# Optimization experiments

Measured on AMD Instinct MI355X. Metric: run time of the kernel, lower is better.

Reference implementation:

```python
import jax, jax.numpy as jnp
import numpy as np

DIM = 2048; N_HEADS = 16; Q_RANK = 1536; KV_RANK = 192
NOPE = 128; ROPE = 64; QK_HD = NOPE + ROPE  # 192 == KV_RANK (required by k_norm/cache widths)
B = 2; S = 2048; MAX_SEQ = 2048
EPS = 1e-6
SCALE = QK_HD ** -0.5


def _rms(v, w):
    return v * jax.lax.rsqrt(jnp.mean(v * v, axis=-1, keepdims=True) + EPS) * w


def _rope(v, cos, sin):
    # v: [..., d] with interleaved (even, odd) pairs, cos/sin broadcastable to [..., d//2]
    vr = v.reshape(v.shape[:-1] + (-1, 2))
    a, b = vr[..., 0], vr[..., 1]
    return jnp.stack([a * cos - b * sin, a * sin + b * cos], axis=-1).reshape(v.shape)


def setup_inputs() -> dict:
    key = jax.random.key(0)
    ks = jax.random.split(key, 8)
    std = 0.02
    x = jax.random.normal(ks[0], (B, S, DIM), jnp.float32)
    # rotary tables: [S, ROPE//2, 2] = (cos, sin)
    t = jnp.arange(S, dtype=jnp.float32)
    inv = 1.0 / (10000.0 ** (jnp.arange(0, ROPE, 2, dtype=jnp.float32) / ROPE))
    ang = jnp.outer(t, inv)
    freqs_cis = jnp.stack([jnp.cos(ang), jnp.sin(ang)], axis=-1)
    mask = jnp.triu(jnp.full((S, S), -1e9, jnp.float32), k=1)  # causal additive mask
    c_kv_cache = jnp.zeros((B, MAX_SEQ, KV_RANK), jnp.float32)
    return {
        "x": x, "start_pos": 0, "freqs_cis": freqs_cis, "mask": mask,
        "c_kv_cache": c_kv_cache,
        "wqa_w": jax.random.normal(ks[1], (Q_RANK, DIM), jnp.float32) * std,
        "wqa_b": jnp.zeros((Q_RANK,), jnp.float32),
        "wqb_w": jax.random.normal(ks[2], (N_HEADS * QK_HD, Q_RANK), jnp.float32) * std,
        "wqb_b": jnp.zeros((N_HEADS * QK_HD,), jnp.float32),
        "q_norm_w": jnp.ones((Q_RANK,), jnp.float32),
        "wkva_w": jax.random.normal(ks[3], (QK_HD, DIM), jnp.float32) * std,
        "wkva_b": jnp.zeros((QK_HD,), jnp.float32),
        "k_norm_w": jnp.ones((KV_RANK,), jnp.float32),
        "wuk_w": jax.random.normal(ks[4], (NOPE, NOPE), jnp.float32) * std,
        "wuk_b": jnp.zeros((NOPE,), jnp.float32),
        "wuv_w": jax.random.normal(ks[5], (DIM, NOPE), jnp.float32) * std,
        "wuv_b": jnp.zeros((DIM,), jnp.float32),
    }


def reference(x, start_pos, freqs_cis, mask, c_kv_cache,
              wqa_w, wqa_b, wqb_w, wqb_b, q_norm_w,
              wkva_w, wkva_b, k_norm_w, wuk_w, wuk_b, wuv_w, wuv_b):
    bsz, seqlen, _ = x.shape
    end = start_pos + seqlen
    cos, sin = freqs_cis[..., 0], freqs_cis[..., 1]  # [seqlen, ROPE//2]

    # low-rank Q path: down-proj -> RMSNorm -> up-proj -> per-head split
    q = _rms(x @ wqa_w.T + wqa_b, q_norm_w)
    q = (q @ wqb_w.T + wqb_b).reshape(bsz, seqlen, N_HEADS, QK_HD)
    q_nope, q_pe = q[..., :NOPE], q[..., NOPE:]
    q_pe = _rope(q_pe, cos[None, :, None, :], sin[None, :, None, :])

    # latent KV path: project -> RMSNorm -> partial RoPE -> scatter into cache
    kv = _rms(x @ wkva_w.T + wkva_b, k_norm_w)  # [b, s, KV_RANK]
    k_pe = _rope(kv[..., NOPE:], cos[None, :, :], sin[None, :, :])
    kv = jnp.concatenate([kv[..., :NOPE], k_pe], axis=-1)
    cache = jax.lax.dynamic_update_slice(c_kv_cache, kv, (0, start_pos, 0))
    keys = cache[:bsz, :end]  # [b, t, KV_RANK]
    k_nope, k_rope = keys[..., :NOPE], keys[..., NOPE:]

    # absorbed attention: fold w_uk into the query side, attend in latent space
    q_abs = q_nope @ wuk_w.T + wuk_b  # [b, s, h, NOPE]
    scores = (jnp.einsum('bshd,btd->bsht', q_abs, k_nope)
              + jnp.einsum('bshr,btr->bsht', q_pe, k_rope)) * SCALE
    scores = scores + mask[None, :seqlen, None, :end]
    attn = jax.nn.softmax(scores, axis=-1)
    out = jnp.einsum('bsht,btd->bshd', attn, k_nope)  # latent values
    out = (out @ wuv_w.T + wuv_b).sum(axis=2)  # up-project values, merge heads -> [b, s, dim]
    return out
```

## Files before the change

### kernel.cpp

```cpp
#include <hip/hip_runtime.h>
#include <hip/hip_bf16.h>
#include <stdint.h>

#define NH     16
#define QRANK  1536
#define NOPE_  128
#define QKHD   192
#define NMERGE 1728
#define B_     2
#define S_     2048
#define MAXSEQ 2048
#define EPS_   1e-6f
#define SCALE_ 0.07216878364870322f

typedef __attribute__((ext_vector_type(4))) float f32x4;
typedef __attribute__((ext_vector_type(8))) short short8;
typedef __attribute__((ext_vector_type(4))) short short4v;

__device__ inline short f2bf(float f){
  uint32_t u = __builtin_bit_cast(uint32_t, f);
  uint32_t r = (u + 0x7FFFu + ((u >> 16) & 1u)) >> 16;
  return (short)(uint16_t)r;
}
__device__ inline float bf2f(short s){
  uint32_t u = ((uint32_t)(uint16_t)s) << 16;
  return __builtin_bit_cast(float, u);
}
__device__ inline void gload16(const short* g, short* l){
  __builtin_amdgcn_global_load_lds((const __attribute__((address_space(1))) void*)g,
                                   (__attribute__((address_space(3))) void*)l, 16, 0, 0);
}

__global__ void k_f2b(const float* __restrict__ in, short* __restrict__ out, long n){
  long i = ((long)blockIdx.x * blockDim.x + threadIdx.x) * 4;
  long stride = (long)gridDim.x * blockDim.x * 4;
  for(; i < n; i += stride){
    float4 v = *reinterpret_cast<const float4*>(in + i);
    short4v o;
    o.x = f2bf(v.x); o.y = f2bf(v.y); o.z = f2bf(v.z); o.w = f2bf(v.w);
    *reinterpret_cast<short4v*>(out + i) = o;
  }
}

template<int BN, bool OUT_BF16>
__global__ __launch_bounds__(256)
void k_gemm97(const short* __restrict__ A, const short* __restrict__ Bm,
              const float* __restrict__ bias, float biasScale,
              void* __restrict__ Cp, int M, int N, int K, int ldc)
{
  constexpr int WN = BN / 2, FN = WN / 16;
  __shared__ short As[128 * 32];
  __shared__ short Bs[BN * 32];
  const int tid = threadIdx.x;
  const int l = tid & 63, w = tid >> 6;
  const int wr = w >> 1, wc = w & 1;
  const long m0 = (long)blockIdx.x * 128;
  const long n0 = (long)blockIdx.y * BN;
  const int lrow = l & 15, lk8 = (l >> 4) * 8;

  int ciA0 = (w*2 + 0)*64 + l, ciA1 = (w*2 + 1)*64 + l;
  const short* a0 = &A[(m0 + (ciA0 >> 2))*(long)K + (ciA0 & 3)*8];
  const short* a1 = &A[(m0 + (ciA1 >> 2))*(long)K + (ciA1 & 3)*8];
  short* lA0 = &As[(w*2 + 0)*512];
  short* lA1 = &As[(w*2 + 1)*512];

  const short* b0; const short* b1 = nullptr;
  short* lB0; short* lB1 = nullptr;
  if constexpr (BN == 128){
    int ciB0 = (w*2 + 0)*64 + l, ciB1 = (w*2 + 1)*64 + l;
    b0 = &Bm[(n0 + (ciB0 >> 2))*(long)K + (ciB0 & 3)*8];
    b1 = &Bm[(n0 + (ciB1 >> 2))*(long)K + (ciB1 & 3)*8];
    lB0 = &Bs[(w*2 + 0)*512];
    lB1 = &Bs[(w*2 + 1)*512];
  } else {
    int ciB = w*64 + l;
    b0 = &Bm[(n0 + (ciB >> 2))*(long)K + (ciB & 3)*8];
    lB0 = &Bs[w*512];
  }

  f32x4 acc[4][FN];
  #pragma unroll
  for(int m = 0; m < 4; m++)
    #pragma unroll
    for(int n = 0; n < FN; n++) acc[m][n] = (f32x4)0.0f;

  for(int kt = 0; kt < K; kt += 32){
    gload16(a0 + kt, lA0);
    gload16(a1 + kt, lA1);
    gload16(b0 + kt, lB0);
    if constexpr (BN == 128) gload16(b1 + kt, lB1);
    __syncthreads();
    short8 af[4], bfv[FN];
    #pragma unroll
    for(int m = 0; m < 4; m++)
      af[m] = *reinterpret_cast<const short8*>(&As[(wr*64 + m*16 + lrow)*32 + lk8]);
    #pragma unroll
    for(int n = 0; n < FN; n++)
      bfv[n] = *reinterpret_cast<const short8*>(&Bs[(wc*WN + n*16 + lrow)*32 + lk8]);
    #pragma unroll
    for(int m = 0; m < 4; m++)
      #pragma unroll
      for(int n = 0; n < FN; n++)
        acc[m][n] = __builtin_amdgcn_mfma_f32_16x16x32_bf16(af[m], bfv[n], acc[m][n], 0, 0, 0);
    __syncthreads();
  }
  #pragma unroll
  for(int m = 0; m < 4; m++){
    int row_l = wr*64 + m*16 + (l >> 4)*4;
    #pragma unroll
    for(int n = 0; n < FN; n++){
      int col = (int)n0 + wc*WN + n*16 + lrow;
      float bv = bias ? bias[col]*biasScale : 0.0f;
      #pragma unroll
      for(int r = 0; r < 4; r++){
        long row = m0 + row_l + r;
        float v = acc[m][n][r] + bv;
        if constexpr (OUT_BF16) ((short*)Cp)[row*(long)ldc + col] = f2bf(v);
        else                    ((float*)Cp)[row*(long)ldc + col] = v;
      }
    }
  }
}

__global__ __launch_bounds__(256)
void k_rms_q(const float* __restrict__ in, const float* __restrict__ bias,
             const float* __restrict__ w, short* __restrict__ out)
{
  const int row = blockIdx.x;
  const int tid = threadIdx.x;
  const float* p = in + (long)row * NMERGE;
  float v[6]; float ss = 0.0f;
  #pragma unroll
  for(int i = 0; i < 6; i++){
    int c = tid + 256*i;
    v[i] = p[c] + bias[c];
    ss += v[i]*v[i];
  }
  #pragma unroll
  for(int off = 1; off < 64; off <<= 1) ss += __shfl_xor(ss, off);
  __shared__ float red[4];
  if((tid & 63) == 0) red[tid >> 6] = ss;
  __syncthreads();
  ss = red[0] + red[1] + red[2] + red[3];
  float scale = rsqrtf(ss / (float)QRANK + EPS_);
  #pragma unroll
  for(int i = 0; i < 6; i++){
    int c = tid + 256*i;
    out[(long)row*QRANK + c] = f2bf(v[i] * scale * w[c]);
  }
}

__global__ __launch_bounds__(256)
void k_qassemble(const short* __restrict__ q, const float* __restrict__ freqs,
                 short* __restrict__ qn, short* __restrict__ qfull)
{
  long idx = (long)blockIdx.x*256 + threadIdx.x;
  long hr = idx / 48; int r = (int)(idx % 48);
  long bs = hr >> 4; int h = (int)(hr & 15);
  int s = (int)(bs & (S_ - 1));
  if(r < 32){
    short4v v = *reinterpret_cast<const short4v*>(&q[bs*3072 + h*QKHD + r*4]);
    *reinterpret_cast<short4v*>(&qn[hr*128 + r*4]) = v;
  } else {
    int c = r - 32;
    short4v v = *reinterpret_cast<const short4v*>(&q[bs*3072 + h*QKHD + 128 + c*4]);
    float a0 = bf2f(v.x), b0 = bf2f(v.y), a1 = bf2f(v.z), b1 = bf2f(v.w);
    int p0 = s*32 + c*2, p1 = p0 + 1;
    float cs0 = freqs[p0*2], sn0 = freqs[p0*2 + 1];
    float cs1 = freqs[p1*2], sn1 = freqs[p1*2 + 1];
    short4v o;
    o.x = f2bf(a0*cs0 - b0*sn0); o.y = f2bf(a0*sn0 + b0*cs0);
    o.z = f2bf(a1*cs1 - b1*sn1); o.w = f2bf(a1*sn1 + b1*cs1);
    *reinterpret_cast<short4v*>(&qfull[hr*QKHD + 128 + c*4]) = o;
  }
}

__global__ __launch_bounds__(256)
void k_kvproc(const float* __restrict__ kvf, const float* __restrict__ kvb,
              const float* __restrict__ w, const float* __restrict__ freqs,
              const float* __restrict__ cache, const int* __restrict__ sp_ptr,
              short* __restrict__ kf)
{
  int wid = threadIdx.x >> 6, l = threadIdx.x & 63;
  long row = (long)blockIdx.x*4 + wid;
  int b = (int)(row >> 11);
  int t = (int)(row & (MAXSEQ - 1));
  int sp = sp_ptr[0];
  int end = sp + S_;
  if(t < sp){
    const float* c = cache + row*QKHD;
    kf[row*QKHD + l]       = f2bf(c[l]);
    kf[row*QKHD + 64 + l]  = f2bf(c[64 + l]);
    kf[row*QKHD + 128 + l] = f2bf(c[128 + l]);
    return;
  }
  if(t >= end) return;
  int s = t - sp;
  const float* p = kvf + ((long)b*S_ + s)*NMERGE;
  float v0 = p[l] + kvb[l];
  float v1 = p[64 + l] + kvb[64 + l];
  float v2 = p[128 + l] + kvb[128 + l];
  float ss = v0*v0 + v1*v1 + v2*v2;
  #pragma unroll
  for(int off = 1; off < 64; off <<= 1) ss += __shfl_xor(ss, off);
  float scale = rsqrtf(ss / (float)QKHD + EPS_);
  float n0 = v0*scale*w[l], n1 = v1*scale*w[64 + l], n2 = v2*scale*w[128 + l];
  kf[row*QKHD + l]      = f2bf(n0);
  kf[row*QKHD + 64 + l] = f2bf(n1);
  int i = l >> 1;
  float cs = freqs[(s*32 + i)*2], sn = freqs[(s*32 + i)*2 + 1];
  float pv = __shfl_xor(n2, 1);
  float r = (l & 1) ? (pv*sn + n2*cs) : (n2*cs - pv*sn);
  kf[row*QKHD + 128 + l] = f2bf(r);
}

__global__ __launch_bounds__(256)
void k_vtrans(const short* __restrict__ kf, short* __restrict__ vt)
{
  __shared__ short T[32 * 132];
  const int b = blockIdx.y;
  const int t0 = blockIdx.x * 32;
  const int tid = threadIdx.x;
  #pragma unroll
  for(int i = 0; i < 4; i++){
    int c = tid + 256*i;
    int tr = c >> 5, dg = c & 31;
    short4v v = *reinterpret_cast<const short4v*>(&kf[((long)b*MAXSEQ + t0 + tr)*QKHD + dg*4]);
    *reinterpret_cast<short4v*>(&T[tr*132 + dg*4]) = v;
  }
  __syncthreads();
  #pragma unroll
  for(int i = 0; i < 4; i++){
    int c = tid + 256*i;
    int dr = c >> 3, tg = c & 7;
    short4v v;
    v.x = T[(tg*4 + 0)*132 + dr];
    v.y = T[(tg*4 + 1)*132 + dr];
    v.z = T[(tg*4 + 2)*132 + dr];
    v.w = T[(tg*4 + 3)*132 + dr];
    *reinterpret_cast<short4v*>(&vt[((long)b*128 + dr)*MAXSEQ + t0 + tg*4]) = v;
  }
}

__global__ __launch_bounds__(256, 4)
void k_attn6(const short* __restrict__ qfull, const short* __restrict__ kf,
             const short* __restrict__ vt, const int* __restrict__ sp_ptr,
             short* __restrict__ oh)
{
  __shared__ short Ks[64 * 192];
  __shared__ short Ps[4][16 * 68];
  const int tid = threadIdx.x;
  const int l = tid & 63, w = tid >> 6;
  const int lrow = l & 15, lhi = l >> 4;
  const int bid = blockIdx.x;
  const int g = bid >> 8, kk = (bid >> 5) & 7, hb = bid & 31;
  const int tile = (g < 2) ? (31 - 8*g - kk) : (8*(3 - g) + kk);
  const int h = hb & 15, b = hb >> 4;
  const int sp = sp_ptr[0];
  const long kbase = (long)b * MAXSEQ;
  const long vbase = (long)b * 128;
  const int q0 = tile * 64;

  short8 kreg[6];

  short8 qa[6];
  {
    int s = q0 + w*16 + lrow;
    const short* qp = qfull + (((long)b*S_ + s)*NH + h)*QKHD + lhi*8;
    #pragma unroll
    for(int ks = 0; ks < 6; ks++) qa[ks] = *reinterpret_cast<const short8*>(qp + ks*32);
  }
  f32x4 o[8];
  #pragma unroll
  for(int df = 0; df < 8; df++) o[df] = (f32x4)0.0f;
  float mrun[4], lrun[4];
  #pragma unroll
  for(int i = 0; i < 4; i++){ mrun[i] = -1e30f; lrun[i] = 0.0f; }

  int hi = q0 + 64 + sp;
  int nt = (hi + 63) >> 6; if(nt > (MAXSEQ >> 6)) nt = MAXSEQ >> 6;

  {
    #pragma unroll
    for(int i = 0; i < 6; i++){
      int cid = tid + 256*i;  int r = cid/24, c = cid%24;
      kreg[i] = *reinterpret_cast<const short8*>(&kf[(kbase + r)*QKHD + c*8]);
    }
    #pragma unroll
    for(int i = 0; i < 6; i++){
      int cid = tid + 256*i;  int r = cid/24, c = cid%24;
      *reinterpret_cast<short8*>(&Ks[r*192 + (c ^ (r & 7))*8]) = kreg[i];
    }
  }
  __syncthreads();

  for(int t0 = 0; t0 < nt; t0++){
    const int T0 = t0 * 64;
    if(t0 + 1 < nt){
      const int Tn = T0 + 64;
      #pragma unroll
      for(int i = 0; i < 6; i++){
        int cid = tid + 256*i;  int r = cid/24, c = cid%24;
        kreg[i] = *reinterpret_cast<const short8*>(&kf[(kbase + Tn + r)*QKHD + c*8]);
      }
    }
    f32x4 sc[4];
    #pragma unroll
    for(int tf = 0; tf < 4; tf++) sc[tf] = (f32x4)0.0f;
    #pragma unroll
    for(int ks = 0; ks < 6; ks++){
      #pragma unroll
      for(int tf = 0; tf < 4; tf++){
        int krow = tf*16 + lrow;
        int cs = (ks*4 + lhi) ^ (lrow & 7);
        short8 bfr = *reinterpret_cast<const short8*>(&Ks[krow*192 + cs*8]);
        sc[tf] = __builtin_amdgcn_mfma_f32_16x16x32_bf16(qa[ks], bfr, sc[tf], 0, 0, 0);
      }
    }
    const bool needmask = (T0 + 63 > q0 + w*16 + sp);
    #pragma unroll
    for(int rr = 0; rr < 4; rr++){
      int q = q0 + w*16 + lhi*4 + rr;
      float s0 = sc[0][rr]*SCALE_, s1 = sc[1][rr]*SCALE_;
      float s2 = sc[2][rr]*SCALE_, s3 = sc[3][rr]*SCALE_;
      if(needmask){
        int t = T0 + lrow;
        if(t      > q + sp) s0 = -1e30f;
        if(t + 16 > q + sp) s1 = -1e30f;
        if(t + 32 > q + sp) s2 = -1e30f;
        if(t + 48 > q + sp) s3 = -1e30f;
      }
      float mx = fmaxf(fmaxf(s0, s1), fmaxf(s2, s3));
      #pragma unroll
      for(int off = 1; off < 16; off <<= 1) mx = fmaxf(mx, __shfl_xor(mx, off));
      if(mx > mrun[rr] + 8.0f){
        float corr = __expf(mrun[rr] - mx);
        lrun[rr] *= corr;
        #pragma unroll
        for(int df = 0; df < 8; df++) o[df][rr] *= corr;
        mrun[rr] = mx;
      }
      float p0 = __expf(s0 - mrun[rr]), p1 = __expf(s1 - mrun[rr]);
      float p2 = __expf(s2 - mrun[rr]), p3 = __expf(s3 - mrun[rr]);
      float psum = (p0 + p1) + (p2 + p3);
      #pragma unroll
      for(int off = 1; off < 16; off <<= 1) psum += __shfl_xor(psum, off);
      lrun[rr] += psum;
      int prow = lhi*4 + rr;
      Ps[w][prow*68 + lrow]      = f2bf(p0);
      Ps[w][prow*68 + 16 + lrow] = f2bf(p1);
      Ps[w][prow*68 + 32 + lrow] = f2bf(p2);
      Ps[w][prow*68 + 48 + lrow] = f2bf(p3);
    }
    short8 pa[2];
    #pragma unroll
    for(int kc = 0; kc < 2; kc++)
      pa[kc] = *reinterpret_cast<const short8*>(&Ps[w][lrow*68 + kc*32 + lhi*8]);
    #pragma unroll
    for(int df = 0; df < 8; df++){
      #pragma unroll
      for(int kc = 0; kc < 2; kc++){
        short8 vfr = *reinterpret_cast<const short8*>(
            &vt[(vbase + df*16 + lrow)*MAXSEQ + T0 + kc*32 + lhi*8]);
        o[df] = __builtin_amdgcn_mfma_f32_16x16x32_bf16(pa[kc], vfr, o[df], 0, 0, 0);
      }
    }
    __syncthreads();
    if(t0 + 1 < nt){
      #pragma unroll
      for(int i = 0; i < 6; i++){
        int cid = tid + 256*i;  int r = cid/24, c = cid%24;
        *reinterpret_cast<short8*>(&Ks[r*192 + (c ^ (r & 7))*8]) = kreg[i];
      }
      __syncthreads();
    }
  }
  #pragma unroll
  for(int rr = 0; rr < 4; rr++){
    int s = q0 + w*16 + lhi*4 + rr;
    float inv = 1.0f / lrun[rr];
    #pragma unroll
    for(int df = 0; df < 8; df++)
      oh[(((long)b*S_ + s)*NH + h)*128 + df*16 + lrow] = f2bf(o[df][rr] * inv);
  }
}

__global__ __launch_bounds__(256)
void k_redheads(const short* __restrict__ ohp, short* __restrict__ hs){
  long idx = (long)blockIdx.x*256 + threadIdx.x;
  long row = idx >> 5; int d4 = (int)(idx & 31);
  float a0 = 0, a1 = 0, a2 = 0, a3 = 0;
  #pragma unroll
  for(int h = 0; h < NH; h++){
    short4v v = *reinterpret_cast<const short4v*>(&ohp[(row*NH + h)*128 + d4*4]);
    a0 += bf2f(v.x); a1 += bf2f(v.y); a2 += bf2f(v.z); a3 += bf2f(v.w);
  }
  short4v o; o.x = f2bf(a0); o.y = f2bf(a1); o.z = f2bf(a2); o.w = f2bf(a3);
  *reinterpret_cast<short4v*>(&hs[row*128 + d4*4]) = o;
}

static constexpr size_t OFF_X16   = 0;
static constexpr size_t OFF_WQAKV = 16777216;
static constexpr size_t OFF_WQB   = 23855104;
static constexpr size_t OFF_WUK   = 33292288;
static constexpr size_t OFF_WUV   = 33325056;
static constexpr size_t OFF_QNORM = 33849344;
static constexpr size_t OFF_QFULL = 46432256;
static constexpr size_t OFF_KFULL = 71598080;
static constexpr size_t OFF_HSUM  = 73170944;
static constexpr size_t OFF_SCR   = 74219520;
static constexpr size_t OFF_QAKV  = OFF_SCR;
static constexpr size_t OFF_Q16   = OFF_SCR;
static constexpr size_t OFF_QN    = OFF_SCR + 25165824;
static constexpr size_t OFF_OH    = OFF_SCR;
static constexpr size_t OFF_VT    = OFF_SCR + 41943040;

extern "C" void kernel_launch(void* const* d_in, const int* in_sizes, int n_in,
                              void* d_out, int out_size, void* d_ws, size_t ws_size,
                              hipStream_t stream)
{
  const float* x      = (const float*)d_in[0];
  const int*   sp     = (const int*)  d_in[1];
  const float* freqs  = (const float*)d_in[2];
  const float* cache  = (const float*)d_in[4];
  const float* wqa_w  = (const float*)d_in[5];
  const float* wqa_b  = (const float*)d_in[6];
  const float* wqb_w  = (const float*)d_in[7];
  const float* wqb_b  = (const float*)d_in[8];
  const float* qnw    = (const float*)d_in[9];
  const float* wkva_w = (const float*)d_in[10];
  const float* wkva_b = (const float*)d_in[11];
  const float* knw    = (const float*)d_in[12];
  const float* wuk_w  = (const float*)d_in[13];
  const float* wuk_b  = (const float*)d_in[14];
  const float* wuv_w  = (const float*)d_in[15];
  const float* wuv_b  = (const float*)d_in[16];

  char* ws = (char*)d_ws;
  short* X16   = (short*)(ws + OFF_X16);
  short* WQAKV = (short*)(ws + OFF_WQAKV);
  short* WQB16 = (short*)(ws + OFF_WQB);
  short* WUK16 = (short*)(ws + OFF_WUK);
  short* WUV16 = (short*)(ws + OFF_WUV);
  short* QNORM = (short*)(ws + OFF_QNORM);
  short* QFULL = (short*)(ws + OFF_QFULL);
  short* KFULL = (short*)(ws + OFF_KFULL);
  short* HSUM  = (short*)(ws + OFF_HSUM);
  float* QAKV  = (float*)(ws + OFF_QAKV);
  short* Q16   = (short*)(ws + OFF_Q16);
  short* QN16  = (short*)(ws + OFF_QN);
  short* OH16  = (short*)(ws + OFF_OH);
  short* VT16  = (short*)(ws + OFF_VT);

  auto cvt = [&](const float* src, short* dst, long n){
    long blocks = (n/4 + 255) / 256; if(blocks > 2048) blocks = 2048;
    k_f2b<<<(int)blocks, 256, 0, stream>>>(src, dst, n);
  };
  cvt(x,      X16,   (long)B_*S_*2048);
  cvt(wqa_w,  WQAKV, (long)QRANK*2048);
  cvt(wkva_w, WQAKV + (long)QRANK*2048, (long)QKHD*2048);
  cvt(wqb_w,  WQB16, (long)NH*QKHD*QRANK);
  cvt(wuk_w,  WUK16, (long)NOPE_*NOPE_);
  cvt(wuv_w,  WUV16, (long)2048*NOPE_);

  k_gemm97<64,false><<<dim3(32,27), 256, 0, stream>>>(X16, WQAKV, nullptr, 0.0f, QAKV, 4096, NMERGE, 2048, NMERGE);
  k_rms_q<<<4096, 256, 0, stream>>>(QAKV, wqa_b, qnw, QNORM);
  k_kvproc<<<1024, 256, 0, stream>>>(QAKV + QRANK, wkva_b, knw, freqs, cache, sp, KFULL);
  k_gemm97<128,true><<<dim3(32,24), 256, 0, stream>>>(QNORM, WQB16, wqb_b, 1.0f, Q16, 4096, NH*QKHD, QRANK, NH*QKHD);
  k_qassemble<<<12288, 256, 0, stream>>>(Q16, freqs, QN16, QFULL);
  k_gemm97<128,true><<<dim3(512,1), 256, 0, stream>>>(QN16, WUK16, wuk_b, 1.0f, QFULL, 65536, 128, 128, QKHD);
  k_vtrans<<<dim3(64,2), 256, 0, stream>>>(KFULL, VT16);
  k_attn6<<<1024, 256, 0, stream>>>(QFULL, KFULL, VT16, sp, OH16);
  k_redheads<<<512, 256, 0, stream>>>(OH16, HSUM);
  k_gemm97<64,false><<<dim3(32,32), 256, 0, stream>>>(HSUM, WUV16, wuv_b, 16.0f, (float*)d_out, 4096, 2048, NOPE_, 2048);
}
```

Measured before the change: 579.5 us.

## Absorb w_uk into keys, pair causal tiles, batch conversions, swizzle GEMM grid

Moves the w_uk projection from the query side (65536 rows) to the key side (4096 rows). Keys become k_nope·W_uk, plus a per-key bias term computed from wuk_b. The QB GEMM now writes straight into QFULL, with rope applied in place, which removes the q-assemble copy. The attention kernel pairs a short and a long causal tile in each block for load balance and stages V through LDS with double-buffered prefetch. It also merges five conversion launches into one and adds an XCD-style block swizzle to the GEMM. The costs are occupancy (launch bounds 3 instead of 4), extra LDS, and two small new kernels.

```diff
diff --git a/kernel.cpp b/kernel.cpp
--- a/kernel.cpp
+++ b/kernel.cpp
@@ -31,22 +31,42 @@
                                    (__attribute__((address_space(3))) void*)l, 16, 0, 0);
 }
 
-__global__ void k_f2b(const float* __restrict__ in, short* __restrict__ out, long n){
+__global__ void k_cvt5(const float* s0, short* d0, long n0,
+                       const float* s1, short* d1, long n1,
+                       const float* s2, short* d2, long n2,
+                       const float* s3, short* d3, long n3,
+                       const float* s4, short* d4, long n4)
+{
+  const float* src; short* dst; long n;
+  switch(blockIdx.y){
+    case 0: src = s0; dst = d0; n = n0; break;
+    case 1: src = s1; dst = d1; n = n1; break;
+    case 2: src = s2; dst = d2; n = n2; break;
+    case 3: src = s3; dst = d3; n = n3; break;
+    default: src = s4; dst = d4; n = n4; break;
+  }
   long i = ((long)blockIdx.x * blockDim.x + threadIdx.x) * 4;
   long stride = (long)gridDim.x * blockDim.x * 4;
   for(; i < n; i += stride){
-    float4 v = *reinterpret_cast<const float4*>(in + i);
+    float4 v = *reinterpret_cast<const float4*>(src + i);
     short4v o;
     o.x = f2bf(v.x); o.y = f2bf(v.y); o.z = f2bf(v.z); o.w = f2bf(v.w);
-    *reinterpret_cast<short4v*>(out + i) = o;
-  }
+    *reinterpret_cast<short4v*>(dst + i) = o;
+  }
+}
+
+__global__ __launch_bounds__(256)
+void k_wukT(const float* __restrict__ wuk, short* __restrict__ wukt){
+  int idx = blockIdx.x*256 + threadIdx.x;
+  int e = idx >> 7, d = idx & 127;
+  wukt[e*128 + d] = f2bf(wuk[d*128 + e]);
 }
 
 template<int BN, bool OUT_BF16>
 __global__ __launch_bounds__(256)
 void k_gemm97(const short* __restrict__ A, const short* __restrict__ Bm,
               const float* __restrict__ bias, float biasScale,
-              void* __restrict__ Cp, int M, int N, int K, int ldc)
+              void* __restrict__ Cp, int lda, int K, int ldc)
 {
   constexpr int WN = BN / 2, FN = WN / 16;
   __shared__ short As[128 * 32];
@@ -54,13 +74,17 @@
   const int tid = threadIdx.x;
   const int l = tid & 63, w = tid >> 6;
   const int wr = w >> 1, wc = w & 1;
-  const long m0 = (long)blockIdx.x * 128;
-  const long n0 = (long)blockIdx.y * BN;
+  int nx = gridDim.x, ny = gridDim.y;
+  int lin = (int)blockIdx.x + nx*(int)blockIdx.y;
+  int nwg = nx*ny;
+  if((nwg & 7) == 0){ int ch = nwg >> 3; lin = (lin & 7)*ch + (lin >> 3); }
+  const long m0 = (long)(lin / ny) * 128;
+  const long n0 = (long)(lin % ny) * BN;
   const int lrow = l & 15, lk8 = (l >> 4) * 8;
 
   int ciA0 = (w*2 + 0)*64 + l, ciA1 = (w*2 + 1)*64 + l;
-  const short* a0 = &A[(m0 + (ciA0 >> 2))*(long)K + (ciA0 & 3)*8];
-  const short* a1 = &A[(m0 + (ciA1 >> 2))*(long)K + (ciA1 & 3)*8];
+  const short* a0 = &A[(m0 + (ciA0 >> 2))*(long)lda + (ciA0 & 3)*8];
+  const short* a1 = &A[(m0 + (ciA1 >> 2))*(long)lda + (ciA1 & 3)*8];
   short* lA0 = &As[(w*2 + 0)*512];
   short* lA1 = &As[(w*2 + 1)*512];
 
@@ -151,28 +175,20 @@
 }
 
 __global__ __launch_bounds__(256)
-void k_qassemble(const short* __restrict__ q, const float* __restrict__ freqs,
-                 short* __restrict__ qn, short* __restrict__ qfull)
-{
+void k_qrope(short* __restrict__ qfull, const float* __restrict__ freqs){
   long idx = (long)blockIdx.x*256 + threadIdx.x;
-  long hr = idx / 48; int r = (int)(idx % 48);
-  long bs = hr >> 4; int h = (int)(hr & 15);
-  int s = (int)(bs & (S_ - 1));
-  if(r < 32){
-    short4v v = *reinterpret_cast<const short4v*>(&q[bs*3072 + h*QKHD + r*4]);
-    *reinterpret_cast<short4v*>(&qn[hr*128 + r*4]) = v;
-  } else {
-    int c = r - 32;
-    short4v v = *reinterpret_cast<const short4v*>(&q[bs*3072 + h*QKHD + 128 + c*4]);
-    float a0 = bf2f(v.x), b0 = bf2f(v.y), a1 = bf2f(v.z), b1 = bf2f(v.w);
-    int p0 = s*32 + c*2, p1 = p0 + 1;
-    float cs0 = freqs[p0*2], sn0 = freqs[p0*2 + 1];
-    float cs1 = freqs[p1*2], sn1 = freqs[p1*2 + 1];
-    short4v o;
-    o.x = f2bf(a0*cs0 - b0*sn0); o.y = f2bf(a0*sn0 + b0*cs0);
-    o.z = f2bf(a1*cs1 - b1*sn1); o.w = f2bf(a1*sn1 + b1*cs1);
-    *reinterpret_cast<short4v*>(&qfull[hr*QKHD + 128 + c*4]) = o;
-  }
+  long row = idx >> 4; int c = (int)(idx & 15);
+  int s = (int)((row >> 4) & (S_ - 1));
+  short* p = &qfull[row*QKHD + 128 + c*4];
+  short4v v = *reinterpret_cast<const short4v*>(p);
+  float a0 = bf2f(v.x), b0 = bf2f(v.y), a1 = bf2f(v.z), b1 = bf2f(v.w);
+  int p0 = s*32 + c*2, p1 = p0 + 1;
+  float cs0 = freqs[p0*2], sn0 = freqs[p0*2 + 1];
+  float cs1 = freqs[p1*2], sn1 = freqs[p1*2 + 1];
+  short4v o;
+  o.x = f2bf(a0*cs0 - b0*sn0); o.y = f2bf(a0*sn0 + b0*cs0);
+  o.z = f2bf(a1*cs1 - b1*sn1); o.w = f2bf(a1*sn1 + b1*cs1);
+  *reinterpret_cast<short4v*>(p) = o;
 }
 
 __global__ __launch_bounds__(256)
@@ -215,6 +231,20 @@
 }
 
 __global__ __launch_bounds__(256)
+void k_kqfin(const short* __restrict__ kf, const float* __restrict__ wukb,
+             short* __restrict__ kq, float* __restrict__ kb)
+{
+  int wid = threadIdx.x >> 6, l = threadIdx.x & 63;
+  long row = (long)blockIdx.x*4 + wid;
+  kq[row*QKHD + 128 + l] = kf[row*QKHD + 128 + l];
+  float acc = bf2f(kf[row*QKHD + 2*l]) * wukb[2*l]
+            + bf2f(kf[row*QKHD + 2*l + 1]) * wukb[2*l + 1];
+  #pragma unroll
+  for(int off = 1; off < 64; off <<= 1) acc += __shfl_xor(acc, off);
+  if(l == 0) kb[row] = acc;
+}
+
+__global__ __launch_bounds__(256)
 void k_vtrans(const short* __restrict__ kf, short* __restrict__ vt)
 {
   __shared__ short T[32 * 132];
@@ -242,146 +272,174 @@
   }
 }
 
-__global__ __launch_bounds__(256, 4)
-void k_attn6(const short* __restrict__ qfull, const short* __restrict__ kf,
-             const short* __restrict__ vt, const int* __restrict__ sp_ptr,
-             short* __restrict__ oh)
+__global__ __launch_bounds__(256, 3)
+void k_attn7(const short* __restrict__ qfull, const short* __restrict__ kq,
+             const short* __restrict__ vtg, const float* __restrict__ kb,
+             const int* __restrict__ sp_ptr, short* __restrict__ oh)
 {
   __shared__ short Ks[64 * 192];
+  __shared__ short Vs[128 * 64];
   __shared__ short Ps[4][16 * 68];
   const int tid = threadIdx.x;
   const int l = tid & 63, w = tid >> 6;
   const int lrow = l & 15, lhi = l >> 4;
-  const int bid = blockIdx.x;
-  const int g = bid >> 8, kk = (bid >> 5) & 7, hb = bid & 31;
-  const int tile = (g < 2) ? (31 - 8*g - kk) : (8*(3 - g) + kk);
-  const int h = hb & 15, b = hb >> 4;
+  const int h = blockIdx.y, b = blockIdx.z;
   const int sp = sp_ptr[0];
   const long kbase = (long)b * MAXSEQ;
   const long vbase = (long)b * 128;
-  const int q0 = tile * 64;
-
-  short8 kreg[6];
-
-  short8 qa[6];
-  {
-    int s = q0 + w*16 + lrow;
-    const short* qp = qfull + (((long)b*S_ + s)*NH + h)*QKHD + lhi*8;
-    #pragma unroll
-    for(int ks = 0; ks < 6; ks++) qa[ks] = *reinterpret_cast<const short8*>(qp + ks*32);
-  }
-  f32x4 o[8];
-  #pragma unroll
-  for(int df = 0; df < 8; df++) o[df] = (f32x4)0.0f;
-  float mrun[4], lrun[4];
-  #pragma unroll
-  for(int i = 0; i < 4; i++){ mrun[i] = -1e30f; lrun[i] = 0.0f; }
-
-  int hi = q0 + 64 + sp;
-  int nt = (hi + 63) >> 6; if(nt > (MAXSEQ >> 6)) nt = MAXSEQ >> 6;
-
-  {
-    #pragma unroll
-    for(int i = 0; i < 6; i++){
-      int cid = tid + 256*i;  int r = cid/24, c = cid%24;
-      kreg[i] = *reinterpret_cast<const short8*>(&kf[(kbase + r)*QKHD + c*8]);
+
+  short8 kreg[6], vreg[4];
+
+  #pragma unroll 1
+  for(int part = 0; part < 2; part++){
+    const int tile = part ? (31 - (int)blockIdx.x) : (int)blockIdx.x;
+    const int q0 = tile * 64;
+
+    short8 qa[6];
+    {
+      int s = q0 + w*16 + lrow;
+      const short* qp = qfull + (((long)b*S_ + s)*NH + h)*QKHD + lhi*8;
+      #pragma unroll
+      for(int ks = 0; ks < 6; ks++) qa[ks] = *reinterpret_cast<const short8*>(qp + ks*32);
     }
-    #pragma unroll
-    for(int i = 0; i < 6; i++){
-      int cid = tid + 256*i;  int r = cid/24, c = cid%24;
-      *reinterpret_cast<short8*>(&Ks[r*192 + (c ^ (r & 7))*8]) = kreg[i];
-    }
-  }
-  __syncthreads();
-
-  for(int t0 = 0; t0 < nt; t0++){
-    const int T0 = t0 * 64;
-    if(t0 + 1 < nt){
-      const int Tn = T0 + 64;
+    f32x4 o[8];
+    #pragma unroll
+    for(int df = 0; df < 8; df++) o[df] = (f32x4)0.0f;
+    float mrun[4], lrun[4];
+    #pragma unroll
+    for(int i = 0; i < 4; i++){ mrun[i] = -1e30f; lrun[i] = 0.0f; }
+
+    int hi = q0 + 64 + sp;
+    int nt = (hi + 63) >> 6; if(nt > (MAXSEQ >> 6)) nt = MAXSEQ >> 6;
+
+    {
       #pragma unroll
       for(int i = 0; i < 6; i++){
         int cid = tid + 256*i;  int r = cid/24, c = cid%24;
-        kreg[i] = *reinterpret_cast<const short8*>(&kf[(kbase + Tn + r)*QKHD + c*8]);
-      }
-    }
-    f32x4 sc[4];
-    #pragma unroll
-    for(int tf = 0; tf < 4; tf++) sc[tf] = (f32x4)0.0f;
-    #pragma unroll
-    for(int ks = 0; ks < 6; ks++){
-      #pragma unroll
-      for(int tf = 0; tf < 4; tf++){
-        int krow = tf*16 + lrow;
-        int cs = (ks*4 + lhi) ^ (lrow & 7);
-        short8 bfr = *reinterpret_cast<const short8*>(&Ks[krow*192 + cs*8]);
-        sc[tf] = __builtin_amdgcn_mfma_f32_16x16x32_bf16(qa[ks], bfr, sc[tf], 0, 0, 0);
-      }
-    }
-    const bool needmask = (T0 + 63 > q0 + w*16 + sp);
-    #pragma unroll
-    for(int rr = 0; rr < 4; rr++){
-      int q = q0 + w*16 + lhi*4 + rr;
-      float s0 = sc[0][rr]*SCALE_, s1 = sc[1][rr]*SCALE_;
-      float s2 = sc[2][rr]*SCALE_, s3 = sc[3][rr]*SCALE_;
-      if(needmask){
-        int t = T0 + lrow;
-        if(t      > q + sp) s0 = -1e30f;
-        if(t + 16 > q + sp) s1 = -1e30f;
-        if(t + 32 > q + sp) s2 = -1e30f;
-        if(t + 48 > q + sp) s3 = -1e30f;
-      }
-      float mx = fmaxf(fmaxf(s0, s1), fmaxf(s2, s3));
-      #pragma unroll
-      for(int off = 1; off < 16; off <<= 1) mx = fmaxf(mx, __shfl_xor(mx, off));
-      if(mx > mrun[rr] + 8.0f){
-        float corr = __expf(mrun[rr] - mx);
-        lrun[rr] *= corr;
-        #pragma unroll
-        for(int df = 0; df < 8; df++) o[df][rr] *= corr;
-        mrun[rr] = mx;
-      }
-      float p0 = __expf(s0 - mrun[rr]), p1 = __expf(s1 - mrun[rr]);
-      float p2 = __expf(s2 - mrun[rr]), p3 = __expf(s3 - mrun[rr]);
-      float psum = (p0 + p1) + (p2 + p3);
-      #pragma unroll
-      for(int off = 1; off < 16; off <<= 1) psum += __shfl_xor(psum, off);
-      lrun[rr] += psum;
-      int prow = lhi*4 + rr;
-      Ps[w][prow*68 + lrow]      = f2bf(p0);
-      Ps[w][prow*68 + 16 + lrow] = f2bf(p1);
-      Ps[w][prow*68 + 32 + lrow] = f2bf(p2);
-      Ps[w][prow*68 + 48 + lrow] = f2bf(p3);
-    }
-    short8 pa[2];
-    #pragma unroll
-    for(int kc = 0; kc < 2; kc++)
-      pa[kc] = *reinterpret_cast<const short8*>(&Ps[w][lrow*68 + kc*32 + lhi*8]);
-    #pragma unroll
-    for(int df = 0; df < 8; df++){
-      #pragma unroll
-      for(int kc = 0; kc < 2; kc++){
-        short8 vfr = *reinterpret_cast<const short8*>(
-            &vt[(vbase + df*16 + lrow)*MAXSEQ + T0 + kc*32 + lhi*8]);
-        o[df] = __builtin_amdgcn_mfma_f32_16x16x32_bf16(pa[kc], vfr, o[df], 0, 0, 0);
-      }
-    }
-    __syncthreads();
-    if(t0 + 1 < nt){
+        kreg[i] = *reinterpret_cast<const short8*>(&kq[(kbase + r)*QKHD + c*8]);
+      }
+      #pragma unroll
+      for(int i = 0; i < 4; i++){
+        int cid = tid + 256*i;  int r = cid >> 3, c = cid & 7;
+        vreg[i] = *reinterpret_cast<const short8*>(&vtg[(vbase + r)*MAXSEQ + c*8]);
+      }
       #pragma unroll
       for(int i = 0; i < 6; i++){
         int cid = tid + 256*i;  int r = cid/24, c = cid%24;
         *reinterpret_cast<short8*>(&Ks[r*192 + (c ^ (r & 7))*8]) = kreg[i];
       }
+      #pragma unroll
+      for(int i = 0; i < 4; i++){
+        int cid = tid + 256*i;  int r = cid >> 3, c = cid & 7;
+        *reinterpret_cast<short8*>(&Vs[r*64 + (c ^ (r & 7))*8]) = vreg[i];
+      }
+    }
+    __syncthreads();
+
+    for(int t0 = 0; t0 < nt; t0++){
+      const int T0 = t0 * 64;
+      if(t0 + 1 < nt){
+        const int Tn = T0 + 64;
+        #pragma unroll
+        for(int i = 0; i < 6; i++){
+          int cid = tid + 256*i;  int r = cid/24, c = cid%24;
+          kreg[i] = *reinterpret_cast<const short8*>(&kq[(kbase + Tn + r)*QKHD + c*8]);
+        }
+        #pragma unroll
+        for(int i = 0; i < 4; i++){
+          int cid = tid + 256*i;  int r = cid >> 3, c = cid & 7;
+          vreg[i] = *reinterpret_cast<const short8*>(&vtg[(vbase + r)*MAXSEQ + Tn + c*8]);
+        }
+      }
+      float kb0 = kb[kbase + T0 + lrow];
+      float kb1 = kb[kbase + T0 + 16 + lrow];
+      float kb2 = kb[kbase + T0 + 32 + lrow];
+      float kb3 = kb[kbase + T0 + 48 + lrow];
+      f32x4 sc[4];
+      #pragma unroll
+      for(int tf = 0; tf < 4; tf++) sc[tf] = (f32x4)0.0f;
+      #pragma unroll
+      for(int ks = 0; ks < 6; ks++){
+        #pragma unroll
+        for(int tf = 0; tf < 4; tf++){
+          int krow = tf*16 + lrow;
+          int cs = (ks*4 + lhi) ^ (lrow & 7);
+          short8 bfr = *reinterpret_cast<const short8*>(&Ks[krow*192 + cs*8]);
+          sc[tf] = __builtin_amdgcn_mfma_f32_16x16x32_bf16(qa[ks], bfr, sc[tf], 0, 0, 0);
+        }
+      }
+      const bool needmask = (T0 + 63 > q0 + w*16 + sp);
+      #pragma unroll
+      for(int rr = 0; rr < 4; rr++){
+        int q = q0 + w*16 + lhi*4 + rr;
+        float s0 = (sc[0][rr] + kb0)*SCALE_, s1 = (sc[1][rr] + kb1)*SCALE_;
+        float s2 = (sc[2][rr] + kb2)*SCALE_, s3 = (sc[3][rr] + kb3)*SCALE_;
+        if(needmask){
+          int t = T0 + lrow;
+          if(t      > q + sp) s0 = -1e30f;
+          if(t + 16 > q + sp) s1 = -1e30f;
+          if(t + 32 > q + sp) s2 = -1e30f;
+          if(t + 48 > q + sp) s3 = -1e30f;
+        }
+        float mx = fmaxf(fmaxf(s0, s1), fmaxf(s2, s3));
+        #pragma unroll
+        for(int off = 1; off < 16; off <<= 1) mx = fmaxf(mx, __shfl_xor(mx, off));
+        if(mx > mrun[rr] + 8.0f){
+          float corr = __expf(mrun[rr] - mx);
+          lrun[rr] *= corr;
+          #pragma unroll
+          for(int df = 0; df < 8; df++) o[df][rr] *= corr;
+          mrun[rr] = mx;
+        }
+        float p0 = __expf(s0 - mrun[rr]), p1 = __expf(s1 - mrun[rr]);
+        float p2 = __expf(s2 - mrun[rr]), p3 = __expf(s3 - mrun[rr]);
+        float psum = (p0 + p1) + (p2 + p3);
+        #pragma unroll
+        for(int off = 1; off < 16; off <<= 1) psum += __shfl_xor(psum, off);
+        lrun[rr] += psum;
+        int prow = lhi*4 + rr;
+        Ps[w][prow*68 + lrow]      = f2bf(p0);
+        Ps[w][prow*68 + 16 + lrow] = f2bf(p1);
+        Ps[w][prow*68 + 32 + lrow] = f2bf(p2);
+        Ps[w][prow*68 + 48 + lrow] = f2bf(p3);
+      }
+      short8 pa[2];
+      #pragma unroll
+      for(int kc = 0; kc < 2; kc++)
+        pa[kc] = *reinterpret_cast<const short8*>(&Ps[w][lrow*68 + kc*32 + lhi*8]);
+      #pragma unroll
+      for(int df = 0; df < 8; df++){
+        #pragma unroll
+        for(int kc = 0; kc < 2; kc++){
+          int vrow = df*16 + lrow;
+          int cs = (kc*4 + lhi) ^ (lrow & 7);
+          short8 vfr = *reinterpret_cast<const short8*>(&Vs[vrow*64 + cs*8]);
+          o[df] = __builtin_amdgcn_mfma_f32_16x16x32_bf16(pa[kc], vfr, o[df], 0, 0, 0);
+        }
+      }
       __syncthreads();
+      if(t0 + 1 < nt){
+        #pragma unroll
+        for(int i = 0; i < 6; i++){
+          int cid = tid + 256*i;  int r = cid/24, c = cid%24;
+          *reinterpret_cast<short8*>(&Ks[r*192 + (c ^ (r & 7))*8]) = kreg[i];
+        }
+        #pragma unroll
+        for(int i = 0; i < 4; i++){
+          int cid = tid + 256*i;  int r = cid >> 3, c = cid & 7;
+          *reinterpret_cast<short8*>(&Vs[r*64 + (c ^ (r & 7))*8]) = vreg[i];
+        }
+        __syncthreads();
+      }
     }
-  }
-  #pragma unroll
-  for(int rr = 0; rr < 4; rr++){
-    int s = q0 + w*16 + lhi*4 + rr;
-    float inv = 1.0f / lrun[rr];
-    #pragma unroll
-    for(int df = 0; df < 8; df++)
-      oh[(((long)b*S_ + s)*NH + h)*128 + df*16 + lrow] = f2bf(o[df][rr] * inv);
+    #pragma unroll
+    for(int rr = 0; rr < 4; rr++){
+      int s = q0 + w*16 + lhi*4 + rr;
+      float inv = 1.0f / lrun[rr];
+      #pragma unroll
+      for(int df = 0; df < 8; df++)
+        oh[(((long)b*S_ + s)*NH + h)*128 + df*16 + lrow] = f2bf(o[df][rr] * inv);
+    }
   }
 }
 
@@ -402,18 +460,18 @@
 static constexpr size_t OFF_X16   = 0;
 static constexpr size_t OFF_WQAKV = 16777216;
 static constexpr size_t OFF_WQB   = 23855104;
-static constexpr size_t OFF_WUK   = 33292288;
+static constexpr size_t OFF_WUKT  = 33292288;
 static constexpr size_t OFF_WUV   = 33325056;
 static constexpr size_t OFF_QNORM = 33849344;
 static constexpr size_t OFF_QFULL = 46432256;
 static constexpr size_t OFF_KFULL = 71598080;
-static constexpr size_t OFF_HSUM  = 73170944;
-static constexpr size_t OFF_SCR   = 74219520;
+static constexpr size_t OFF_KQ    = 73170944;
+static constexpr size_t OFF_KB    = 74743808;
+static constexpr size_t OFF_VT    = 74760192;
+static constexpr size_t OFF_HSUM  = 75808768;
+static constexpr size_t OFF_SCR   = 76857344;
 static constexpr size_t OFF_QAKV  = OFF_SCR;
-static constexpr size_t OFF_Q16   = OFF_SCR;
-static constexpr size_t OFF_QN    = OFF_SCR + 25165824;
 static constexpr size_t OFF_OH    = OFF_SCR;
-static constexpr size_t OFF_VT    = OFF_SCR + 41943040;
 
 extern "C" void kernel_launch(void* const* d_in, const int* in_sizes, int n_in,
                               void* d_out, int out_size, void* d_ws, size_t ws_size,
@@ -440,37 +498,35 @@
   short* X16   = (short*)(ws + OFF_X16);
   short* WQAKV = (short*)(ws + OFF_WQAKV);
   short* WQB16 = (short*)(ws + OFF_WQB);
-  short* WUK16 = (short*)(ws + OFF_WUK);
+  short* WUKT  = (short*)(ws + OFF_WUKT);
   short* WUV16 = (short*)(ws + OFF_WUV);
   short* QNORM = (short*)(ws + OFF_QNORM);
   short* QFULL = (short*)(ws + OFF_QFULL);
   short* KFULL = (short*)(ws + OFF_KFULL);
+  short* KQ    = (short*)(ws + OFF_KQ);
+  float* KB    = (float*)(ws + OFF_KB);
+  short* VT16  = (short*)(ws + OFF_VT);
   short* HSUM  = (short*)(ws + OFF_HSUM);
   float* QAKV  = (float*)(ws + OFF_QAKV);
-  short* Q16   = (short*)(ws + OFF_Q16);
-  short* QN16  = (short*)(ws + OFF_QN);
   short* OH16  = (short*)(ws + OFF_OH);
-  short* VT16  = (short*)(ws + OFF_VT);
-
-  auto cvt = [&](const float* src, short* dst, long n){
-    long blocks = (n/4 + 255) / 256; if(blocks > 2048) blocks = 2048;
-    k_f2b<<<(int)blocks, 256, 0, stream>>>(src, dst, n);
-  };
-  cvt(x,      X16,   (long)B_*S_*2048);
-  cvt(wqa_w,  WQAKV, (long)QRANK*2048);
-  cvt(wkva_w, WQAKV + (long)QRANK*2048, (long)QKHD*2048);
-  cvt(wqb_w,  WQB16, (long)NH*QKHD*QRANK);
-  cvt(wuk_w,  WUK16, (long)NOPE_*NOPE_);
-  cvt(wuv_w,  WUV16, (long)2048*NOPE_);
-
-  k_gemm97<64,false><<<dim3(32,27), 256, 0, stream>>>(X16, WQAKV, nullptr, 0.0f, QAKV, 4096, NMERGE, 2048, NMERGE);
+
+  k_cvt5<<<dim3(1024,5), 256, 0, stream>>>(
+      x,      X16,                         (long)B_*S_*2048,
+      wqa_w,  WQAKV,                       (long)QRANK*2048,
+      wkva_w, WQAKV + (long)QRANK*2048,    (long)QKHD*2048,
+      wqb_w,  WQB16,                       (long)NH*QKHD*QRANK,
+      wuv_w,  WUV16,                       (long)2048*NOPE_);
+  k_wukT<<<64, 256, 0, stream>>>(wuk_w, WUKT);
+
+  k_gemm97<64,false><<<dim3(32,27), 256, 0, stream>>>(X16, WQAKV, nullptr, 0.0f, QAKV, 2048, 2048, NMERGE);
   k_rms_q<<<4096, 256, 0, stream>>>(QAKV, wqa_b, qnw, QNORM);
   k_kvproc<<<1024, 256, 0, stream>>>(QAKV + QRANK, wkva_b, knw, freqs, cache, sp, KFULL);
-  k_gemm97<128,true><<<dim3(32,24), 256, 0, stream>>>(QNORM, WQB16, wqb_b, 1.0f, Q16, 4096, NH*QKHD, QRANK, NH*QKHD);
-  k_qassemble<<<12288, 256, 0, stream>>>(Q16, freqs, QN16, QFULL);
-  k_gemm97<128,true><<<dim3(512,1), 256, 0, stream>>>(QN16, WUK16, wuk_b, 1.0f, QFULL, 65536, 128, 128, QKHD);
+  k_gemm97<128,true><<<dim3(32,24), 256, 0, stream>>>(QNORM, WQB16, wqb_b, 1.0f, QFULL, QRANK, QRANK, NH*QKHD);
+  k_qrope<<<4096, 256, 0, stream>>>(QFULL, freqs);
+  k_gemm97<128,true><<<dim3(32,1), 256, 0, stream>>>(KFULL, WUKT, nullptr, 0.0f, KQ, QKHD, NOPE_, QKHD);
+  k_kqfin<<<1024, 256, 0, stream>>>(KFULL, wuk_b, KQ, KB);
   k_vtrans<<<dim3(64,2), 256, 0, stream>>>(KFULL, VT16);
-  k_attn6<<<1024, 256, 0, stream>>>(QFULL, KFULL, VT16, sp, OH16);
+  k_attn7<<<dim3(16,16,2), 256, 0, stream>>>(QFULL, KQ, VT16, KB, sp, OH16);
   k_redheads<<<512, 256, 0, stream>>>(OH16, HSUM);
-  k_gemm97<64,false><<<dim3(32,32), 256, 0, stream>>>(HSUM, WUV16, wuv_b, 16.0f, (float*)d_out, 4096, 2048, NOPE_, 2048);
-}
+  k_gemm97<64,false><<<dim3(32,32), 256, 0, stream>>>(HSUM, WUV16, wuv_b, 16.0f, (float*)d_out, NOPE_, NOPE_, 2048);
+}
```

Result: faster. 471.6 us (-18.6%).
